# Kernel tuning notes

Measured on AMD Instinct MI355X. Metric: run time of the kernel, lower is better.

Reference implementation:

```python
import jax, jax.numpy as jnp
import numpy as np

NEG_SLOPE = 0.2  # PyG GATConv default


def gat_conv(x, src, dst, W, a_src, a_dst, bias, n):
    # x: [N, Fin] -> h: [N, Fout]
    h = x @ W
    alpha_s = h @ a_src  # [N]
    alpha_d = h @ a_dst  # [N]
    e = jax.nn.leaky_relu(alpha_s[src] + alpha_d[dst], NEG_SLOPE)  # [E]
    # segment softmax over incoming edges of each target node
    m = jax.ops.segment_max(e, dst, num_segments=n)
    e = jnp.exp(e - m[dst])
    denom = jax.ops.segment_sum(e, dst, num_segments=n)
    alpha = e / denom[dst]
    out = jax.ops.segment_sum(alpha[:, None] * h[src], dst, num_segments=n)
    return out + bias


def setup_inputs() -> dict:
    key = jax.random.key(0)
    ks = jax.random.split(key, 10)
    N, E, FIN, HID, FOUT = 100000, 3200000, 128, 32, 64
    x = jax.random.normal(ks[0], (N, FIN), dtype=jnp.float32)
    edge_index = jax.random.randint(ks[1], (2, E), 0, N, dtype=jnp.int64)
    s = 1.0 / np.sqrt(FIN)
    W1 = jax.random.normal(ks[2], (FIN, HID), dtype=jnp.float32) * s
    a1_src = jax.random.normal(ks[3], (HID,), dtype=jnp.float32) * 0.1
    a1_dst = jax.random.normal(ks[4], (HID,), dtype=jnp.float32) * 0.1
    b1 = jnp.zeros((HID,), dtype=jnp.float32)
    W2 = jax.random.normal(ks[5], (HID, FOUT), dtype=jnp.float32) * (1.0 / np.sqrt(HID))
    a2_src = jax.random.normal(ks[6], (FOUT,), dtype=jnp.float32) * 0.1
    a2_dst = jax.random.normal(ks[7], (FOUT,), dtype=jnp.float32) * 0.1
    b2 = jnp.zeros((FOUT,), dtype=jnp.float32)
    return {"x": x, "edge_index": edge_index, "W1": W1, "a1_src": a1_src,
            "a1_dst": a1_dst, "b1": b1, "W2": W2, "a2_src": a2_src,
            "a2_dst": a2_dst, "b2": b2}


def reference(x, edge_index, W1, a1_src, a1_dst, b1, W2, a2_src, a2_dst, b2):
    n = x.shape[0]
    # add self loops (GATConv default add_self_loops=True)
    loop = jnp.arange(n, dtype=edge_index.dtype)
    src = jnp.concatenate([edge_index[0], loop])
    dst = jnp.concatenate([edge_index[1], loop])
    h = gat_conv(x, src, dst, W1, a1_src, a1_dst, b1, n)
    h = jax.nn.relu(h)
    out = gat_conv(h, src, dst, W2, a2_src, a2_dst, b2, n)
    return out
```

## Files before the change

### kernel.cpp

```cpp
#include <hip/hip_runtime.h>
#include <cstdint>
#include <cmath>

#define NEG_SLOPE 0.2f
#define BSH 6
#define CSH 9
#define CBN 512
#define RATIO 8
#define PCHUNK 8192

__device__ __forceinline__ float leaky(float v) { return v > 0.f ? v : NEG_SLOPE * v; }
__device__ __forceinline__ float uf(unsigned u) { return __uint_as_float(u); }

__device__ __forceinline__ unsigned short f2bf(float f) {
    unsigned u = __float_as_uint(f);
    unsigned r = ((u >> 16) & 1u) + 0x7fffu;
    return (unsigned short)((u + r) >> 16);
}
__device__ __forceinline__ float bflo(unsigned q) { return __uint_as_float(q << 16); }
__device__ __forceinline__ float bfhi(unsigned q) { return __uint_as_float(q & 0xffff0000u); }

template <int FIN, int FOUT, int CPR, int LCPR>
__global__ __launch_bounds__(256, 4) void gemm_rows(
    const float* __restrict__ X, const float* __restrict__ W,
    const float* __restrict__ a_src, const float* __restrict__ a_dst,
    unsigned short* __restrict__ H, float* __restrict__ As, float* __restrict__ Ad,
    float* __restrict__ bmax, int N)
{
    constexpr int ROWS = 256 / CPR;
    constexpr int XST = FIN + 4;
    static_assert((1 << LCPR) == CPR && CPR * 4 == FOUT, "geometry");

    __shared__ float Ws[FIN * FOUT];
    __shared__ float Xs[ROWS * XST];
    __shared__ float wmax[4];

    const int tid = threadIdx.x;
    const int base = blockIdx.x * ROWS;

    for (int i = tid; i < FIN * FOUT / 4; i += 256)
        reinterpret_cast<float4*>(Ws)[i] = reinterpret_cast<const float4*>(W)[i];

    for (int i = tid; i < ROWS * FIN / 4; i += 256) {
        int row = i / (FIN / 4);
        int k4 = (i - row * (FIN / 4)) * 4;
        float4 v = make_float4(0.f, 0.f, 0.f, 0.f);
        if (base + row < N)
            v = *reinterpret_cast<const float4*>(&X[(size_t)(base + row) * FIN + k4]);
        *reinterpret_cast<float4*>(&Xs[row * XST + k4]) = v;
    }
    __syncthreads();

    const int colg = tid & (CPR - 1);
    const int row = tid >> LCPR;
    const int c0 = colg * 4;

    float4 acc = make_float4(0.f, 0.f, 0.f, 0.f);

#pragma unroll 2
    for (int k = 0; k < FIN; k += 4) {
        float4 xv = *reinterpret_cast<const float4*>(&Xs[row * XST + k]);
        float4 w0 = *reinterpret_cast<const float4*>(&Ws[(k + 0) * FOUT + c0]);
        float4 w1 = *reinterpret_cast<const float4*>(&Ws[(k + 1) * FOUT + c0]);
        float4 w2 = *reinterpret_cast<const float4*>(&Ws[(k + 2) * FOUT + c0]);
        float4 w3 = *reinterpret_cast<const float4*>(&Ws[(k + 3) * FOUT + c0]);
        acc.x = fmaf(xv.w, w3.x, fmaf(xv.z, w2.x, fmaf(xv.y, w1.x, fmaf(xv.x, w0.x, acc.x))));
        acc.y = fmaf(xv.w, w3.y, fmaf(xv.z, w2.y, fmaf(xv.y, w1.y, fmaf(xv.x, w0.y, acc.y))));
        acc.z = fmaf(xv.w, w3.z, fmaf(xv.z, w2.z, fmaf(xv.y, w1.z, fmaf(xv.x, w0.z, acc.z))));
        acc.w = fmaf(xv.w, w3.w, fmaf(xv.z, w2.w, fmaf(xv.y, w1.w, fmaf(xv.x, w0.w, acc.w))));
    }

    const int grow = base + row;
    if (grow < N) {
        ushort4 hv;
        hv.x = f2bf(acc.x); hv.y = f2bf(acc.y);
        hv.z = f2bf(acc.z); hv.w = f2bf(acc.w);
        *reinterpret_cast<ushort4*>(&H[(size_t)grow * FOUT + c0]) = hv;
    }

    float4 asv = *reinterpret_cast<const float4*>(&a_src[c0]);
    float4 adv = *reinterpret_cast<const float4*>(&a_dst[c0]);
    float ps = acc.x * asv.x + acc.y * asv.y + acc.z * asv.z + acc.w * asv.w;
    float pd = acc.x * adv.x + acc.y * adv.y + acc.z * adv.z + acc.w * adv.w;
#pragma unroll
    for (int ofs = 1; ofs < CPR; ofs <<= 1) {
        ps += __shfl_xor(ps, ofs);
        pd += __shfl_xor(pd, ofs);
    }
    if (colg == 0 && grow < N) { As[grow] = ps; Ad[grow] = pd; }

    float pm = (grow < N) ? ps : -3.0e38f;
#pragma unroll
    for (int ofs = 1; ofs < 64; ofs <<= 1) pm = fmaxf(pm, __shfl_xor(pm, ofs));
    if ((tid & 63) == 0) wmax[tid >> 6] = pm;
    __syncthreads();
    if (tid == 0)
        bmax[blockIdx.x] = fmaxf(fmaxf(wmax[0], wmax[1]), fmaxf(wmax[2], wmax[3]));
}

__global__ __launch_bounds__(256) void reduce_max_kernel(
    const float* __restrict__ bmax, int nb, float* __restrict__ gmax)
{
    __shared__ float sd[256];
    const int t = threadIdx.x;
    float m = -3.0e38f;
    for (int i = t; i < nb; i += 256) m = fmaxf(m, bmax[i]);
    sd[t] = m; __syncthreads();
    for (int ofs = 128; ofs; ofs >>= 1) {
        if (t < ofs) sd[t] = fmaxf(sd[t], sd[t + ofs]);
        __syncthreads();
    }
    if (t == 0) *gmax = sd[0];
}

__global__ __launch_bounds__(256) void chunk_hist(
    const int* __restrict__ dst, int* __restrict__ pcT,
    int E, int NB, int NCC, int NCH)
{
    __shared__ int hc[2048];
    const int t = threadIdx.x;
    for (int i = t; i < 2048; i += 256) hc[i] = 0;
    __syncthreads();
    const int base = blockIdx.x * PCHUNK;
    const int end = (base + PCHUNK < E) ? base + PCHUNK : E;
    for (int e = base + t; e < end; e += 256)
        atomicAdd(&hc[dst[e] >> BSH], 1);
    __syncthreads();
    if (t < NCC) {
        int f0 = t * RATIO;
        int s = 0;
#pragma unroll
        for (int j = 0; j < RATIO; ++j) {
            int fb = f0 + j;
            if (fb < NB) s += hc[fb];
        }
        pcT[(size_t)t * NCH + blockIdx.x] = s;
    }
}

__global__ __launch_bounds__(256) void coarse_total(
    const int* __restrict__ pcT, int* __restrict__ totals, int NCH)
{
    __shared__ int sd[256];
    const int t = threadIdx.x;
    int s = 0;
    for (int i = t; i < NCH; i += 256)
        s += pcT[(size_t)blockIdx.x * NCH + i];
    sd[t] = s; __syncthreads();
    for (int ofs = 128; ofs; ofs >>= 1) {
        if (t < ofs) sd[t] += sd[t + ofs];
        __syncthreads();
    }
    if (t == 0) totals[blockIdx.x] = sd[0];
}

__global__ __launch_bounds__(256) void boffc_scan(
    const int* __restrict__ totals, int* __restrict__ boffC, int NCC)
{
    __shared__ int sd[256];
    const int t = threadIdx.x;
    int v = (t < NCC) ? totals[t] : 0;
    sd[t] = v; __syncthreads();
    for (int ofs = 1; ofs < 256; ofs <<= 1) {
        int tmp = (t >= ofs) ? sd[t - ofs] : 0;
        __syncthreads();
        sd[t] += tmp;
        __syncthreads();
    }
    if (t < NCC) boffC[t] = sd[t] - v;
    if (t == 255) boffC[NCC] = sd[255];
}

__global__ __launch_bounds__(256) void coarse_scan(
    const int* __restrict__ pcT, const int* __restrict__ boffC,
    int* __restrict__ co, int NCH)
{
    __shared__ int sd[256];
    const int c = blockIdx.x;
    const int t = threadIdx.x;
    const int base = boffC[c];
    int carry = 0;
    for (int start = 0; start < NCH; start += 256) {
        int idx = start + t;
        int v = (idx < NCH) ? pcT[(size_t)c * NCH + idx] : 0;
        sd[t] = v; __syncthreads();
        for (int ofs = 1; ofs < 256; ofs <<= 1) {
            int tmp = (t >= ofs) ? sd[t - ofs] : 0;
            __syncthreads();
            sd[t] += tmp;
            __syncthreads();
        }
        int incl = sd[t];
        int total = sd[255];
        if (idx < NCH) co[(size_t)idx * 256 + c] = base + carry + incl - v;
        carry += total;
        __syncthreads();
    }
}

__global__ __launch_bounds__(256) void coarse_partition(
    const int* __restrict__ src, const int* __restrict__ dst,
    const int* __restrict__ co, int* __restrict__ csrA, int E, int NCC)
{
    __shared__ int lcur[256], gpos[256];
    const int t = threadIdx.x;
    lcur[t] = 0;
    if (t < NCC) gpos[t] = co[(size_t)blockIdx.x * 256 + t];
    __syncthreads();
    const int base = blockIdx.x * PCHUNK;
    int bb[32], pp[32];
#pragma unroll
    for (int i = 0; i < 32; ++i) {
        int e = base + i * 256 + t;
        bb[i] = -1;
        if (e < E) {
            int sv = src[e], dv = dst[e];
            bb[i] = dv >> CSH;
            pp[i] = (sv << CSH) | (dv & (CBN - 1));
        }
    }
#pragma unroll
    for (int i = 0; i < 32; ++i) {
        if (bb[i] >= 0) {
            int b = bb[i];
            csrA[gpos[b] + atomicAdd(&lcur[b], 1)] = pp[i];
        }
    }
}

__global__ __launch_bounds__(256) void node_sort(
    const int* __restrict__ csrA, const int* __restrict__ boffC,
    int* __restrict__ off, int* __restrict__ csr, int N, int NCC, int E)
{
    __shared__ int cnt[CBN];
    __shared__ int pref[CBN];
    __shared__ int sd[256];
    const int c = blockIdx.x;
    const int t = threadIdx.x;
    const int p0 = boffC[c];
    const int p1 = boffC[c + 1];
    const int n0 = c << CSH;

    for (int i = t; i < CBN; i += 256) cnt[i] = 0;
    __syncthreads();
    for (int i = p0 + t; i < p1; i += 256)
        atomicAdd(&cnt[csrA[i] & (CBN - 1)], 1);
    __syncthreads();
    int a0 = cnt[2 * t], a1 = cnt[2 * t + 1];
    int pairsum = a0 + a1;
    sd[t] = pairsum; __syncthreads();
    for (int ofs = 1; ofs < 256; ofs <<= 1) {
        int tmp = (t >= ofs) ? sd[t - ofs] : 0;
        __syncthreads();
        sd[t] += tmp;
        __syncthreads();
    }
    int run = sd[t] - pairsum;
    pref[2 * t] = run;
    pref[2 * t + 1] = run + a0;
    int n = n0 + 2 * t;
    if (n < N) off[n] = p0 + run;
    if (n + 1 < N) off[n + 1] = p0 + run + a0;
    if (c == NCC - 1 && t == 0) off[N] = E;
    __syncthreads();
    for (int i = t; i < CBN; i += 256) cnt[i] = 0;
    __syncthreads();
    for (int i = p0 + t; i < p1; i += 256) {
        int v = csrA[i];
        int ln = v & (CBN - 1);
        int p = atomicAdd(&cnt[ln], 1);
        csr[p0 + pref[ln] + p] = v >> CSH;
    }
}

template <int F, bool RELU>
__global__ __launch_bounds__(256) void gat_aggregate(
    const int* __restrict__ csr, const int* __restrict__ off,
    const float* __restrict__ As, const float* __restrict__ Ad,
    const unsigned short* __restrict__ Hb, const float* __restrict__ bias,
    const float* __restrict__ gmax, float* __restrict__ Out, int N)
{
    constexpr int LPR = F / 4;
    constexpr int EPI = 64 / LPR;
    constexpr unsigned RB = F * 2;

    __shared__ uint2 pr[4][64];
    const int wave = threadIdx.x >> 6;
    const int lane = threadIdx.x & 63;
    const int n = blockIdx.x * 4 + wave;
    if (n >= N) return;

    const int o0 = off[n];
    const int deg = off[n + 1] - o0;
    const float adn = Ad[n];
    const float eself = leaky(As[n] + adn);
    const float m = leaky(*gmax + adn);

    uint2* myp = pr[wave];
    const char* Hc = (const char*)Hb;
    const int subg = lane / LPR;
    const unsigned f8 = (unsigned)(lane & (LPR - 1)) * 8u;

    float4 acc = make_float4(0.f, 0.f, 0.f, 0.f);
    float denp = 0.f;

    for (int c = 0; c < deg; c += 64) {
        int i = c + lane;
        float w = 0.f; unsigned sb = 0;
        if (i < deg) {
            int s = csr[o0 + i];
            w = __expf(leaky(As[s] + adn) - m);
            sb = (unsigned)s * RB;
            denp += w;
        }
        myp[lane] = make_uint2(sb, __float_as_uint(w));
        int lim = (deg - c < 64) ? deg - c : 64;
        int j = subg;
        for (; j + 3 * EPI < lim; j += 4 * EPI) {
            uint2 p0 = myp[j], p1 = myp[j + EPI], p2 = myp[j + 2 * EPI], p3 = myp[j + 3 * EPI];
            uint2 q0 = *(const uint2*)(Hc + p0.x + f8);
            uint2 q1 = *(const uint2*)(Hc + p1.x + f8);
            uint2 q2 = *(const uint2*)(Hc + p2.x + f8);
            uint2 q3 = *(const uint2*)(Hc + p3.x + f8);
            float w0 = uf(p0.y), w1 = uf(p1.y), w2 = uf(p2.y), w3 = uf(p3.y);
            acc.x = fmaf(w0, bflo(q0.x), acc.x); acc.y = fmaf(w0, bfhi(q0.x), acc.y);
            acc.z = fmaf(w0, bflo(q0.y), acc.z); acc.w = fmaf(w0, bfhi(q0.y), acc.w);
            acc.x = fmaf(w1, bflo(q1.x), acc.x); acc.y = fmaf(w1, bfhi(q1.x), acc.y);
            acc.z = fmaf(w1, bflo(q1.y), acc.z); acc.w = fmaf(w1, bfhi(q1.y), acc.w);
            acc.x = fmaf(w2, bflo(q2.x), acc.x); acc.y = fmaf(w2, bfhi(q2.x), acc.y);
            acc.z = fmaf(w2, bflo(q2.y), acc.z); acc.w = fmaf(w2, bfhi(q2.y), acc.w);
            acc.x = fmaf(w3, bflo(q3.x), acc.x); acc.y = fmaf(w3, bfhi(q3.x), acc.y);
            acc.z = fmaf(w3, bflo(q3.y), acc.z); acc.w = fmaf(w3, bfhi(q3.y), acc.w);
        }
        for (; j < lim; j += EPI) {
            uint2 p = myp[j];
            uint2 q = *(const uint2*)(Hc + p.x + f8);
            float w0 = uf(p.y);
            acc.x = fmaf(w0, bflo(q.x), acc.x); acc.y = fmaf(w0, bfhi(q.x), acc.y);
            acc.z = fmaf(w0, bflo(q.y), acc.z); acc.w = fmaf(w0, bfhi(q.y), acc.w);
        }
    }

#pragma unroll
    for (int ofs = 32; ofs >= LPR; ofs >>= 1) {
        acc.x += __shfl_xor(acc.x, ofs);
        acc.y += __shfl_xor(acc.y, ofs);
        acc.z += __shfl_xor(acc.z, ofs);
        acc.w += __shfl_xor(acc.w, ofs);
    }
#pragma unroll
    for (int ofs = 1; ofs < 64; ofs <<= 1) denp += __shfl_xor(denp, ofs);

    float wsf = __expf(eself - m);
    uint2 qs = *(const uint2*)(Hc + (size_t)n * RB + f8);
    acc.x = fmaf(wsf, bflo(qs.x), acc.x); acc.y = fmaf(wsf, bfhi(qs.x), acc.y);
    acc.z = fmaf(wsf, bflo(qs.y), acc.z); acc.w = fmaf(wsf, bfhi(qs.y), acc.w);
    float den = denp + wsf;

    if (subg == 0) {
        int fi = (lane & (LPR - 1)) * 4;
        float4 bv = *reinterpret_cast<const float4*>(&bias[fi]);
        float4 v;
        v.x = acc.x / den + bv.x;
        v.y = acc.y / den + bv.y;
        v.z = acc.z / den + bv.z;
        v.w = acc.w / den + bv.w;
        if (RELU) {
            v.x = fmaxf(v.x, 0.f); v.y = fmaxf(v.y, 0.f);
            v.z = fmaxf(v.z, 0.f); v.w = fmaxf(v.w, 0.f);
        }
        *reinterpret_cast<float4*>(&Out[(size_t)n * F + fi]) = v;
    }
}

extern "C" void kernel_launch(void* const* d_in, const int* in_sizes, int n_in,
                              void* d_out, int out_size, void* d_ws, size_t ws_size,
                              hipStream_t stream)
{
    const float* x   = (const float*)d_in[0];
    const int*   ei  = (const int*)d_in[1];
    const float* W1  = (const float*)d_in[2];
    const float* a1s = (const float*)d_in[3];
    const float* a1d = (const float*)d_in[4];
    const float* b1  = (const float*)d_in[5];
    const float* W2  = (const float*)d_in[6];
    const float* a2s = (const float*)d_in[7];
    const float* a2d = (const float*)d_in[8];
    const float* b2  = (const float*)d_in[9];

    const int N = in_sizes[0] / 128;
    const int E = in_sizes[1] / 2;
    const int NB = (N + 63) >> BSH;
    const int NCC = (N + CBN - 1) >> CSH;
    const int NCH = (E + PCHUNK - 1) / PCHUNK;
    const int* src = ei;
    const int* dst = ei + E;
    float* out = (float*)d_out;

    const int g1 = (N + 31) / 32;
    const int g2 = (N + 15) / 16;

    float* ws = (float*)d_ws;
    size_t o = 0;
    unsigned short* h1b = (unsigned short*)(ws + o); o += (size_t)N * 16;
    float* h1a = ws + o; o += (size_t)N * 32;
    unsigned short* h2b = (unsigned short*)(ws + o); o += (size_t)N * 32;
    float* as1 = ws + o; o += N;
    float* ad1 = ws + o; o += N;
    float* as2 = ws + o; o += N;
    float* ad2 = ws + o; o += N;
    float* bmax = ws + o; o += (size_t)g2;
    float* gmax1 = ws + o; o += 1;
    float* gmax2 = ws + o; o += 1;
    int* ip = (int*)(ws + o);
    size_t io = 0;
    int* pcT    = ip + io; io += (size_t)NCC * NCH;
    int* totals = ip + io; io += NCC;
    int* boffC  = ip + io; io += (NCC + 1);
    int* co     = ip + io; io += (size_t)NCH * 256;
    int* off    = ip + io; io += (N + 1);
    int* csrA   = ip + io; io += E;
    int* csr    = ip + io; io += E;


    chunk_hist<<<NCH, 256, 0, stream>>>(dst, pcT, E, NB, NCC, NCH);
    coarse_total<<<NCC, 256, 0, stream>>>(pcT, totals, NCH);
    boffc_scan<<<1, 256, 0, stream>>>(totals, boffC, NCC);
    coarse_scan<<<NCC, 256, 0, stream>>>(pcT, boffC, co, NCH);
    coarse_partition<<<NCH, 256, 0, stream>>>(src, dst, co, csrA, E, NCC);
    node_sort<<<NCC, 256, 0, stream>>>(csrA, boffC, off, csr, N, NCC, E);

    const int gn = (N + 3) / 4;

    gemm_rows<128, 32, 8, 3><<<g1, 256, 0, stream>>>(
        x, W1, a1s, a1d, h1b, as1, ad1, bmax, N);
    reduce_max_kernel<<<1, 256, 0, stream>>>(bmax, g1, gmax1);
    gat_aggregate<32, true><<<gn, 256, 0, stream>>>(
        csr, off, as1, ad1, h1b, b1, gmax1, h1a, N);

    gemm_rows<32, 64, 16, 4><<<g2, 256, 0, stream>>>(
        h1a, W2, a2s, a2d, h2b, as2, ad2, bmax, N);
    reduce_max_kernel<<<1, 256, 0, stream>>>(bmax, g2, gmax2);
    gat_aggregate<64, false><<<gn, 256, 0, stream>>>(
        csr, off, as2, ad2, h2b, b2, gmax2, out, N);
}
```

Before: 265.3 us.

## Aggregate layer-2 in 32-dim input space and apply W2 after aggregation

Uses linearity to reorder layer 2 as sum(alpha * h1[src]) @ W2, so it gathers 32-wide bf16 rows of h1 instead of 64-wide projected rows. The attention scores are computed directly from h1 using precomputed W2·a vectors. The separate layer-2 GEMM is removed, and each wave multiplies its aggregated vector by W2, which is staged in shared memory. This halves the per-edge gather bytes in layer 2, at the cost of an extra fp32 copy of h1, a small per-node matvec, and 8KB of shared memory per block that may reduce occupancy.

New measurement: 257.0 us. 3.1% less time.

```diff
diff --git a/kernel.cpp b/kernel.cpp
--- a/kernel.cpp
+++ b/kernel.cpp
@@ -113,6 +113,48 @@
     if (t == 0) *gmax = sd[0];
 }
 
+__global__ __launch_bounds__(64) void w2prep(
+    const float* __restrict__ W2, const float* __restrict__ a2s,
+    const float* __restrict__ a2d, float* __restrict__ w2s, float* __restrict__ w2d)
+{
+    const int t = threadIdx.x;
+    const int i = t & 31;
+    const float* a = (t < 32) ? a2s : a2d;
+    float s = 0.f;
+    for (int j = 0; j < 64; ++j) s = fmaf(W2[i * 64 + j], a[j], s);
+    if (t < 32) w2s[i] = s; else w2d[i] = s;
+}
+
+__global__ __launch_bounds__(256) void alpha2_kernel(
+    const float* __restrict__ h1f, const float* __restrict__ w2s,
+    const float* __restrict__ w2d, float* __restrict__ As2, float* __restrict__ Ad2,
+    float* __restrict__ bmaxa, int N)
+{
+    __shared__ float wmax[4];
+    const int tid = threadIdx.x;
+    const int n = blockIdx.x * 256 + tid;
+    float ps = 0.f, pd = 0.f;
+    if (n < N) {
+        const float4* p = reinterpret_cast<const float4*>(h1f + (size_t)n * 32);
+#pragma unroll
+        for (int w = 0; w < 8; ++w) {
+            float4 v = p[w];
+            ps = fmaf(v.x, w2s[4 * w + 0], ps); ps = fmaf(v.y, w2s[4 * w + 1], ps);
+            ps = fmaf(v.z, w2s[4 * w + 2], ps); ps = fmaf(v.w, w2s[4 * w + 3], ps);
+            pd = fmaf(v.x, w2d[4 * w + 0], pd); pd = fmaf(v.y, w2d[4 * w + 1], pd);
+            pd = fmaf(v.z, w2d[4 * w + 2], pd); pd = fmaf(v.w, w2d[4 * w + 3], pd);
+        }
+        As2[n] = ps; Ad2[n] = pd;
+    }
+    float pm = (n < N) ? ps : -3.0e38f;
+#pragma unroll
+    for (int ofs = 1; ofs < 64; ofs <<= 1) pm = fmaxf(pm, __shfl_xor(pm, ofs));
+    if ((tid & 63) == 0) wmax[tid >> 6] = pm;
+    __syncthreads();
+    if (tid == 0)
+        bmaxa[blockIdx.x] = fmaxf(fmaxf(wmax[0], wmax[1]), fmaxf(wmax[2], wmax[3]));
+}
+
 __global__ __launch_bounds__(256) void chunk_hist(
     const int* __restrict__ dst, int* __restrict__ pcT,
     int E, int NB, int NCC, int NCH)
@@ -273,16 +315,16 @@
     }
 }
 
-template <int F, bool RELU>
-__global__ __launch_bounds__(256) void gat_aggregate(
+__global__ __launch_bounds__(256) void gat_agg1(
     const int* __restrict__ csr, const int* __restrict__ off,
     const float* __restrict__ As, const float* __restrict__ Ad,
     const unsigned short* __restrict__ Hb, const float* __restrict__ bias,
-    const float* __restrict__ gmax, float* __restrict__ Out, int N)
-{
-    constexpr int LPR = F / 4;
-    constexpr int EPI = 64 / LPR;
-    constexpr unsigned RB = F * 2;
+    const float* __restrict__ gmax, unsigned short* __restrict__ Out,
+    float* __restrict__ OutF, int N)
+{
+    constexpr int LPR = 8;
+    constexpr int EPI = 8;
+    constexpr unsigned RB = 64;
 
     __shared__ uint2 pr[4][64];
     const int wave = threadIdx.x >> 6;
@@ -360,17 +402,118 @@
     if (subg == 0) {
         int fi = (lane & (LPR - 1)) * 4;
         float4 bv = *reinterpret_cast<const float4*>(&bias[fi]);
-        float4 v;
-        v.x = acc.x / den + bv.x;
-        v.y = acc.y / den + bv.y;
-        v.z = acc.z / den + bv.z;
-        v.w = acc.w / den + bv.w;
-        if (RELU) {
-            v.x = fmaxf(v.x, 0.f); v.y = fmaxf(v.y, 0.f);
-            v.z = fmaxf(v.z, 0.f); v.w = fmaxf(v.w, 0.f);
-        }
-        *reinterpret_cast<float4*>(&Out[(size_t)n * F + fi]) = v;
-    }
+        float vx = fmaxf(acc.x / den + bv.x, 0.f);
+        float vy = fmaxf(acc.y / den + bv.y, 0.f);
+        float vz = fmaxf(acc.z / den + bv.z, 0.f);
+        float vw = fmaxf(acc.w / den + bv.w, 0.f);
+        ushort4 hv;
+        hv.x = f2bf(vx); hv.y = f2bf(vy); hv.z = f2bf(vz); hv.w = f2bf(vw);
+        *reinterpret_cast<ushort4*>(&Out[(size_t)n * 32 + fi]) = hv;
+        *reinterpret_cast<float4*>(&OutF[(size_t)n * 32 + fi]) =
+            make_float4(vx, vy, vz, vw);
+    }
+}
+
+__global__ __launch_bounds__(256) void gat_agg2(
+    const int* __restrict__ csr, const int* __restrict__ off,
+    const float* __restrict__ As, const float* __restrict__ Ad,
+    const unsigned short* __restrict__ Hb, const float* __restrict__ W2,
+    const float* __restrict__ b2, const float* __restrict__ gmax,
+    float* __restrict__ Out, int N)
+{
+    constexpr int LPR = 8;
+    constexpr int EPI = 8;
+    constexpr unsigned RB = 64;
+
+    __shared__ float Ws2[32 * 64];
+    __shared__ uint2 pr[4][64];
+    __shared__ float aggv[4][32];
+
+    const int tid = threadIdx.x;
+    for (int i = tid; i < 32 * 64 / 4; i += 256)
+        reinterpret_cast<float4*>(Ws2)[i] = reinterpret_cast<const float4*>(W2)[i];
+    __syncthreads();
+
+    const int wave = tid >> 6;
+    const int lane = tid & 63;
+    const int n = blockIdx.x * 4 + wave;
+    if (n >= N) return;
+
+    const int o0 = off[n];
+    const int deg = off[n + 1] - o0;
+    const float adn = Ad[n];
+    const float eself = leaky(As[n] + adn);
+    const float m = leaky(*gmax + adn);
+
+    uint2* myp = pr[wave];
+    const char* Hc = (const char*)Hb;
+    const int subg = lane / LPR;
+    const unsigned f8 = (unsigned)(lane & (LPR - 1)) * 8u;
+
+    float4 acc = make_float4(0.f, 0.f, 0.f, 0.f);
+    float denp = 0.f;
+
+    for (int c = 0; c < deg; c += 64) {
+        int i = c + lane;
+        float w = 0.f; unsigned sb = 0;
+        if (i < deg) {
+            int s = csr[o0 + i];
+            w = __expf(leaky(As[s] + adn) - m);
+            sb = (unsigned)s * RB;
+            denp += w;
+        }
+        myp[lane] = make_uint2(sb, __float_as_uint(w));
+        int lim = (deg - c < 64) ? deg - c : 64;
+        int j = subg;
+        for (; j + 3 * EPI < lim; j += 4 * EPI) {
+            uint2 p0 = myp[j], p1 = myp[j + EPI], p2 = myp[j + 2 * EPI], p3 = myp[j + 3 * EPI];
+            uint2 q0 = *(const uint2*)(Hc + p0.x + f8);
+            uint2 q1 = *(const uint2*)(Hc + p1.x + f8);
+            uint2 q2 = *(const uint2*)(Hc + p2.x + f8);
+            uint2 q3 = *(const uint2*)(Hc + p3.x + f8);
+            float w0 = uf(p0.y), w1 = uf(p1.y), w2 = uf(p2.y), w3 = uf(p3.y);
+            acc.x = fmaf(w0, bflo(q0.x), acc.x); acc.y = fmaf(w0, bfhi(q0.x), acc.y);
+            acc.z = fmaf(w0, bflo(q0.y), acc.z); acc.w = fmaf(w0, bfhi(q0.y), acc.w);
+            acc.x = fmaf(w1, bflo(q1.x), acc.x); acc.y = fmaf(w1, bfhi(q1.x), acc.y);
+            acc.z = fmaf(w1, bflo(q1.y), acc.z); acc.w = fmaf(w1, bfhi(q1.y), acc.w);
+            acc.x = fmaf(w2, bflo(q2.x), acc.x); acc.y = fmaf(w2, bfhi(q2.x), acc.y);
+            acc.z = fmaf(w2, bflo(q2.y), acc.z); acc.w = fmaf(w2, bfhi(q2.y), acc.w);
+            acc.x = fmaf(w3, bflo(q3.x), acc.x); acc.y = fmaf(w3, bfhi(q3.x), acc.y);
+            acc.z = fmaf(w3, bflo(q3.y), acc.z); acc.w = fmaf(w3, bfhi(q3.y), acc.w);
+        }
+        for (; j < lim; j += EPI) {
+            uint2 p = myp[j];
+            uint2 q = *(const uint2*)(Hc + p.x + f8);
+            float w0 = uf(p.y);
+            acc.x = fmaf(w0, bflo(q.x), acc.x); acc.y = fmaf(w0, bfhi(q.x), acc.y);
+            acc.z = fmaf(w0, bflo(q.y), acc.z); acc.w = fmaf(w0, bfhi(q.y), acc.w);
+        }
+    }
+
+#pragma unroll
+    for (int ofs = 32; ofs >= LPR; ofs >>= 1) {
+        acc.x += __shfl_xor(acc.x, ofs);
+        acc.y += __shfl_xor(acc.y, ofs);
+        acc.z += __shfl_xor(acc.z, ofs);
+        acc.w += __shfl_xor(acc.w, ofs);
+    }
+#pragma unroll
+    for (int ofs = 1; ofs < 64; ofs <<= 1) denp += __shfl_xor(denp, ofs);
+
+    float wsf = __expf(eself - m);
+    uint2 qs = *(const uint2*)(Hc + (size_t)n * RB + f8);
+    acc.x = fmaf(wsf, bflo(qs.x), acc.x); acc.y = fmaf(wsf, bfhi(qs.x), acc.y);
+    acc.z = fmaf(wsf, bflo(qs.y), acc.z); acc.w = fmaf(wsf, bfhi(qs.y), acc.w);
+    float den = denp + wsf;
+
+    if (subg == 0)
+        *reinterpret_cast<float4*>(&aggv[wave][(lane & (LPR - 1)) * 4]) = acc;
+
+    float s = 0.f;
+#pragma unroll
+    for (int k = 0; k < 32; ++k)
+        s = fmaf(aggv[wave][k], Ws2[k * 64 + lane], s);
+    Out[(size_t)n * 64 + lane] = s / den + b2[lane];
 }
 
 extern "C" void kernel_launch(void* const* d_in, const int* in_sizes, int n_in,
@@ -398,20 +541,23 @@
     float* out = (float*)d_out;
 
     const int g1 = (N + 31) / 32;
-    const int g2 = (N + 15) / 16;
+    const int ga = (N + 255) / 256;
 
     float* ws = (float*)d_ws;
     size_t o = 0;
     unsigned short* h1b = (unsigned short*)(ws + o); o += (size_t)N * 16;
-    float* h1a = ws + o; o += (size_t)N * 32;
-    unsigned short* h2b = (unsigned short*)(ws + o); o += (size_t)N * 32;
+    unsigned short* h1a = (unsigned short*)(ws + o); o += (size_t)N * 16;
+    float* h1f = ws + o; o += (size_t)N * 32;
     float* as1 = ws + o; o += N;
     float* ad1 = ws + o; o += N;
     float* as2 = ws + o; o += N;
     float* ad2 = ws + o; o += N;
-    float* bmax = ws + o; o += (size_t)g2;
+    float* bmax = ws + o; o += (size_t)g1;
+    float* bmaxa = ws + o; o += (size_t)ga;
     float* gmax1 = ws + o; o += 1;
     float* gmax2 = ws + o; o += 1;
+    float* w2s = ws + o; o += 32;
+    float* w2d = ws + o; o += 32;
     int* ip = (int*)(ws + o);
     size_t io = 0;
     int* pcT    = ip + io; io += (size_t)NCC * NCH;
@@ -422,7 +568,6 @@
     int* csrA   = ip + io; io += E;
     int* csr    = ip + io; io += E;
 
-
     chunk_hist<<<NCH, 256, 0, stream>>>(dst, pcT, E, NB, NCC, NCH);
     coarse_total<<<NCC, 256, 0, stream>>>(pcT, totals, NCH);
     boffc_scan<<<1, 256, 0, stream>>>(totals, boffC, NCC);
@@ -435,12 +580,12 @@
     gemm_rows<128, 32, 8, 3><<<g1, 256, 0, stream>>>(
         x, W1, a1s, a1d, h1b, as1, ad1, bmax, N);
     reduce_max_kernel<<<1, 256, 0, stream>>>(bmax, g1, gmax1);
-    gat_aggregate<32, true><<<gn, 256, 0, stream>>>(
-        csr, off, as1, ad1, h1b, b1, gmax1, h1a, N);
-
-    gemm_rows<32, 64, 16, 4><<<g2, 256, 0, stream>>>(
-        h1a, W2, a2s, a2d, h2b, as2, ad2, bmax, N);
-    reduce_max_kernel<<<1, 256, 0, stream>>>(bmax, g2, gmax2);
-    gat_aggregate<64, false><<<gn, 256, 0, stream>>>(
-        csr, off, as2, ad2, h2b, b2, gmax2, out, N);
-}
+    gat_agg1<<<gn, 256, 0, stream>>>(
+        csr, off, as1, ad1, h1b, b1, gmax1, h1a, h1f, N);
+
+    w2prep<<<1, 64, 0, stream>>>(W2, a2s, a2d, w2s, w2d);
+    alpha2_kernel<<<ga, 256, 0, stream>>>(h1f, w2s, w2d, as2, ad2, bmaxa, N);
+    reduce_max_kernel<<<1, 256, 0, stream>>>(bmaxa, ga, gmax2);
+    gat_agg2<<<gn, 256, 0, stream>>>(
+        csr, off, as2, ad2, h1a, W2, b2, gmax2, out, N);
+}
```
